# Kernel optimization log

Hardware: AMD Instinct MI355X
Metric: run time of the kernel (lower is better)

The kernel has to match this reference:

```python
import jax, jax.numpy as jnp
import numpy as np

AUDIO_DIM = 256
VIDEO_DIM = 256
CONV_CH = 128
FUSED_DIM = 512
EPS = 1e-12


def _interp_linear(x, t_out):
    # x: [B, T_in, D]; torch F.interpolate(mode='linear', align_corners=False)
    t_in = x.shape[1]
    scale = t_in / t_out
    src = (jnp.arange(t_out, dtype=jnp.float32) + 0.5) * scale - 0.5
    src = jnp.maximum(src, 0.0)
    i0 = jnp.floor(src).astype(jnp.int32)
    i0 = jnp.minimum(i0, t_in - 1)
    i1 = jnp.minimum(i0 + 1, t_in - 1)
    w = (src - i0.astype(jnp.float32))[None, :, None]
    return x[:, i0, :] * (1.0 - w) + x[:, i1, :] * w


def _conv1d(x, w, b, pad):
    # x: [B, C, T], w: [O, I, K]
    y = jax.lax.conv_general_dilated(x, w, window_strides=(1,), padding=[(pad, pad)],
                                     dimension_numbers=('NCH', 'OIH', 'NCH'))
    return y + b[None, :, None]


def setup_inputs() -> dict:
    key = jax.random.key(0)
    ks = jax.random.split(key, 12)
    B, Ta, Tv = 16, 2048, 1024

    def xavier(k, shape):
        fan_out, fan_in = shape[0], int(np.prod(shape[1:]))
        std = float(np.sqrt(2.0 / (fan_in + fan_out)))
        return jax.random.normal(k, shape, dtype=jnp.float32) * std

    return {
        'audio_features': jax.random.normal(ks[0], (B, Ta, AUDIO_DIM), dtype=jnp.float32),
        'video_features': jax.random.normal(ks[1], (B, Tv, VIDEO_DIM), dtype=jnp.float32),
        'a3_w': xavier(ks[2], (CONV_CH, AUDIO_DIM, 3)), 'a3_b': jnp.zeros((CONV_CH,), jnp.float32),
        'a5_w': xavier(ks[3], (CONV_CH, AUDIO_DIM, 5)), 'a5_b': jnp.zeros((CONV_CH,), jnp.float32),
        'v3_w': xavier(ks[4], (CONV_CH, VIDEO_DIM, 3)), 'v3_b': jnp.zeros((CONV_CH,), jnp.float32),
        'v5_w': xavier(ks[5], (CONV_CH, VIDEO_DIM, 5)), 'v5_b': jnp.zeros((CONV_CH,), jnp.float32),
        'proj_w': xavier(ks[6], (FUSED_DIM, FUSED_DIM)), 'proj_b': jnp.zeros((FUSED_DIM,), jnp.float32),
    }


def reference(audio_features, video_features, a3_w, a3_b, a5_w, a5_b,
              v3_w, v3_b, v5_w, v5_b, proj_w, proj_b):
    Ta, Tv = audio_features.shape[1], video_features.shape[1]
    T = max((Ta + Tv) // 2, 1)
    # temporal alignment to common length T
    a = _interp_linear(audio_features, T)  # [B, T, 256]
    v = _interp_linear(video_features, T)  # [B, T, 256]

    gelu = lambda x: jax.nn.gelu(x, approximate=False)
    a_in = jnp.swapaxes(a, 1, 2)  # [B, 256, T]
    v_in = jnp.swapaxes(v, 1, 2)
    a_multi = jnp.concatenate([gelu(_conv1d(a_in, a3_w, a3_b, 1)),
                               gelu(_conv1d(a_in, a5_w, a5_b, 2))], axis=1)  # [B, 256, T]
    v_multi = jnp.concatenate([gelu(_conv1d(v_in, v3_w, v3_b, 1)),
                               gelu(_conv1d(v_in, v5_w, v5_b, 2))], axis=1)
    a_multi = jnp.swapaxes(a_multi, 1, 2)  # [B, T, 256]
    v_multi = jnp.swapaxes(v_multi, 1, 2)

    # cosine-similarity cross attention (torch F.normalize eps=1e-12)
    a_norm = a_multi / jnp.maximum(jnp.linalg.norm(a_multi, axis=-1, keepdims=True), EPS)
    v_norm = v_multi / jnp.maximum(jnp.linalg.norm(v_multi, axis=-1, keepdims=True), EPS)
    sim = jnp.einsum('btd,bsd->bts', a_norm, v_norm)  # [B, T, T]

    attn_a2v = jax.nn.softmax(sim, axis=-1)              # audio attends video
    attn_v2a = jnp.swapaxes(jax.nn.softmax(sim, axis=1), 1, 2)  # video attends audio
    a_enh = jnp.einsum('bts,bsd->btd', attn_a2v, v_multi)
    v_enh = jnp.einsum('bst,btd->bsd', jnp.swapaxes(attn_v2a, 1, 2), a_multi)
    # (equivalently v_enh = attn_v2a @ a_multi)
    v_enh = jnp.einsum('bts,bsd->btd', attn_v2a, a_multi)

    fused = jnp.concatenate([a + a_enh, v + v_enh], axis=-1)  # [B, T, 512]
    out = gelu(fused @ proj_w.T + proj_b)
    # dropout is identity in eval mode
    return out
```

## Files before the change

### kernel.cpp

```cpp
#include <hip/hip_runtime.h>
#include <math.h>

#define BATCH 16
#define TA 2048
#define TV 1024
#define TT 1536
#define DIM 256
#define FD 512

typedef unsigned short u16;
typedef unsigned int u32;
typedef short bf16x8 __attribute__((ext_vector_type(8)));
typedef float f32x4 __attribute__((ext_vector_type(4)));

__device__ __forceinline__ float bf2f(u16 u) {
  union { u32 i; float f; } v; v.i = ((u32)u) << 16; return v.f;
}
__device__ __forceinline__ u16 f2bf(float f) {
  union { float f; u32 i; } v; v.f = f;
  return (u16)((v.i + 0x7fffu + ((v.i >> 16) & 1u)) >> 16);
}
__device__ __forceinline__ float gelu_f(float x) {
  return 0.5f * x * (1.0f + erff(x * 0.70710678118654752440f));
}
__device__ __forceinline__ void async16(const u16* g, u16* l) {
  __builtin_amdgcn_global_load_lds((const __attribute__((address_space(1))) void*)g,
                                   (__attribute__((address_space(3))) void*)l, 16, 0, 0);
}

__global__ __launch_bounds__(256) void k_prep(
    const float* __restrict__ a3w, const float* __restrict__ a5w,
    const float* __restrict__ v3w, const float* __restrict__ v5w,
    const float* __restrict__ pw,
    u16* __restrict__ w3a, u16* __restrict__ w5a,
    u16* __restrict__ w3v, u16* __restrict__ w5v, u16* __restrict__ wp) {
  int idx = blockIdx.x * 256 + threadIdx.x;
  if (idx < 524288) {
    int e, ktaps;
    const float* src;
    u16* dst;
    if (idx < 98304)       { e = idx;          ktaps = 3; src = a3w; dst = w3a; }
    else if (idx < 262144) { e = idx - 98304;  ktaps = 5; src = a5w; dst = w5a; }
    else if (idx < 360448) { e = idx - 262144; ktaps = 3; src = v3w; dst = w3v; }
    else                   { e = idx - 360448; ktaps = 5; src = v5w; dst = w5v; }
    int kk = e >> 12, r = e & 4095;
    int j = r & 7, unit = r >> 3;
    int fb = unit >> 6, rem = unit & 63;
    int q = rem >> 4, colp = rem & 15;
    int o = fb * 16 + colp;
    int tap = kk >> 3;
    int c = (kk & 7) * 32 + q * 8 + j;
    dst[e] = f2bf(src[(o * 256 + c) * ktaps + tap]);
  } else if (idx < 786432) {
    int t = idx - 524288;
    wp[t] = f2bf(pw[t]);
  }
}

__global__ __launch_bounds__(256) void k_interp(const float* __restrict__ in,
                                                u16* __restrict__ out,
                                                int t_in, float scale) {
  int b = blockIdx.y;
  int i = blockIdx.x * 256 + threadIdx.x;
  int t = i >> 5, dg = i & 31;
  float src = ((float)t + 0.5f) * scale - 0.5f;
  src = fmaxf(src, 0.0f);
  int i0 = (int)floorf(src);
  if (i0 > t_in - 1) i0 = t_in - 1;
  int i1 = i0 + 1; if (i1 > t_in - 1) i1 = t_in - 1;
  float w = src - (float)i0;
  float om = 1.0f - w;
  const float4* p0 = (const float4*)(in + ((size_t)(b * t_in + i0)) * DIM + dg * 8);
  const float4* p1 = (const float4*)(in + ((size_t)(b * t_in + i1)) * DIM + dg * 8);
  float4 x0a = p0[0], x0b = p0[1], x1a = p1[0], x1b = p1[1];
  u16 r[8];
  r[0] = f2bf(x0a.x * om + x1a.x * w); r[1] = f2bf(x0a.y * om + x1a.y * w);
  r[2] = f2bf(x0a.z * om + x1a.z * w); r[3] = f2bf(x0a.w * om + x1a.w * w);
  r[4] = f2bf(x0b.x * om + x1b.x * w); r[5] = f2bf(x0b.y * om + x1b.y * w);
  r[6] = f2bf(x0b.z * om + x1b.z * w); r[7] = f2bf(x0b.w * om + x1b.w * w);
  u32 w0 = (u32)r[0] | ((u32)r[1] << 16), w1 = (u32)r[2] | ((u32)r[3] << 16);
  u32 w2 = (u32)r[4] | ((u32)r[5] << 16), w3 = (u32)r[6] | ((u32)r[7] << 16);
  *(uint4*)(out + ((size_t)(b * TT + t)) * DIM + dg * 8) = make_uint4(w0, w1, w2, w3);
}

__global__ __launch_bounds__(256) void k_zero(float* __restrict__ p, int n) {
  int i = blockIdx.x * 256 + threadIdx.x;
  if (i < n) p[i] = 0.f;
}

template <int TAPS>
__global__ __launch_bounds__(256) void k_convN(
    const u16* __restrict__ xa, const u16* __restrict__ xv,
    const u16* __restrict__ Wa, const u16* __restrict__ Wv,
    const float* __restrict__ ba, const float* __restrict__ bv,
    u16* __restrict__ outMa, u16* __restrict__ outMv,
    u16* __restrict__ outTa, u16* __restrict__ outTv,
    float* __restrict__ nsqa, float* __restrict__ nsqv) {
  constexpr int S = TAPS * 8;
  constexpr int OFF = (TAPS == 3) ? 1 : 2;
  constexpr int CHB = (TAPS == 3) ? 0 : 128;
  __shared__ __align__(16) u16 xs[68 * 264];
  __shared__ __align__(16) u16 Bs[2 * 4096];
  u16* tb = xs;
  int b = blockIdx.y, t0 = blockIdx.x * 64;
  int isv = blockIdx.z;
  const u16* xin = isv ? xv : xa;
  const u16* W   = isv ? Wv : Wa;
  const float* bias = isv ? bv : ba;
  u16* outM  = isv ? outMv : outMa;
  u16* outT  = isv ? outTv : outTa;
  float* nsq = isv ? nsqv : nsqa;
  int tid = threadIdx.x, wave = tid >> 6, lane = tid & 63;
  int col = lane & 15, quad = lane >> 4;

  for (int i = tid; i < 68 * 32; i += 256) {
    int row = i >> 5, un = i & 31;
    int t = t0 + row - 2;
    uint4 val = make_uint4(0, 0, 0, 0);
    if (t >= 0 && t < TT) val = *(const uint4*)(xin + ((size_t)(b * TT + t)) * DIM + un * 8);
    *(uint4*)(xs + row * 264 + un * 8) = val;
  }
  const u16* Wb = W + wave * 1024 + lane * 8;
  u16* BsW = Bs + wave * 1024;
  async16(Wb, BsW);
  async16(Wb + 512, BsW + 512);

  f32x4 acc[4][2];
  f32x4 zz = {0.f, 0.f, 0.f, 0.f};
#pragma unroll
  for (int rt = 0; rt < 4; rt++) { acc[rt][0] = zz; acc[rt][1] = zz; }

  const u16* afp = xs + (col + 2) * 264 + quad * 8;
  const u16* bfp = Bs + wave * 1024 + quad * 128 + col * 8;

#pragma unroll
  for (int s = 0; s < S; s++) {
    __syncthreads();
    if (s + 1 < S) {
      const u16* src = Wb + (size_t)(s + 1) * 4096;
      u16* dst = Bs + ((s + 1) & 1) * 4096 + wave * 1024;
      async16(src, dst);
      async16(src + 512, dst + 512);
    }
    constexpr int dummy = 0; (void)dummy;
    int shift = (s >> 3) - OFF;
    int c0 = (s & 7) * 32;
    bf16x8 af[4];
#pragma unroll
    for (int rt = 0; rt < 4; rt++)
      af[rt] = *(const bf16x8*)(afp + (rt * 16 + shift) * 264 + c0);
    bf16x8 bf0 = *(const bf16x8*)(bfp + (s & 1) * 4096);
    bf16x8 bf1 = *(const bf16x8*)(bfp + (s & 1) * 4096 + 512);
#pragma unroll
    for (int rt = 0; rt < 4; rt++) {
      acc[rt][0] = __builtin_amdgcn_mfma_f32_16x16x32_bf16(af[rt], bf0, acc[rt][0], 0, 0, 0);
      acc[rt][1] = __builtin_amdgcn_mfma_f32_16x16x32_bf16(af[rt], bf1, acc[rt][1], 0, 0, 0);
    }
  }
  __syncthreads();

  float bia0 = bias[wave * 32 + col];
  float bia1 = bias[wave * 32 + 16 + col];
  float ss[4][4];
#pragma unroll
  for (int rt = 0; rt < 4; rt++)
#pragma unroll
    for (int r = 0; r < 4; r++) ss[rt][r] = 0.f;
#pragma unroll
  for (int rt = 0; rt < 4; rt++)
#pragma unroll
    for (int h = 0; h < 2; h++) {
      float bia = h ? bia1 : bia0;
      int chL = wave * 32 + h * 16 + col;
#pragma unroll
      for (int r = 0; r < 4; r++) {
        float g = gelu_f(acc[rt][h][r] + bia);
        ss[rt][r] += g * g;
        int trow = rt * 16 + quad * 4 + r;
        u16 gb = f2bf(g);
        tb[chL * 72 + trow] = gb;
        outM[((size_t)(b * TT + t0 + trow)) * DIM + CHB + chL] = gb;
      }
    }
#pragma unroll
  for (int rt = 0; rt < 4; rt++)
#pragma unroll
    for (int r = 0; r < 4; r++) {
      float v = ss[rt][r];
      v += __shfl_xor(v, 1, 64); v += __shfl_xor(v, 2, 64);
      v += __shfl_xor(v, 4, 64); v += __shfl_xor(v, 8, 64);
      if (col == 0)
        atomicAdd(&nsq[b * TT + t0 + rt * 16 + quad * 4 + r], v);
    }
  __syncthreads();
  {
    int ch = tid >> 1, half = tid & 1;
    uint4* dst = (uint4*)(outT + ((size_t)(b * 256 + CHB + ch)) * TT + t0 + half * 32);
#pragma unroll
    for (int i = 0; i < 4; i++)
      dst[i] = *(const uint4*)(tb + ch * 72 + half * 32 + i * 8);
  }
}

__global__ __launch_bounds__(256) void k_sim(const u16* __restrict__ A,
                                             const u16* __restrict__ Bm,
                                             const float* __restrict__ naq,
                                             const float* __restrict__ nvq,
                                             u16* __restrict__ E,
                                             u16* __restrict__ ET,
                                             float* __restrict__ rsum,
                                             float* __restrict__ csum) {
  __shared__ u16 As[128 * 32], Bs[128 * 32];
  __shared__ float sRa[128], sRv[128];
  int b = blockIdx.z, m0 = blockIdx.y * 128, n0 = blockIdx.x * 128;
  int tid = threadIdx.x, wave = tid >> 6, lane = tid & 63;
  int col = lane & 15, quad = lane >> 4;
  int wm = (wave >> 1) * 64, wn = (wave & 1) * 64;
  int lrow = lane >> 2, lcol = (lane & 3) * 8;
  if (tid < 128) sRa[tid] = 1.0f / fmaxf(sqrtf(naq[b * TT + m0 + tid]), 1e-12f);
  else sRv[tid - 128] = 1.0f / fmaxf(sqrtf(nvq[b * TT + tid - 128 + n0]), 1e-12f);
  const u16* Ab = A + ((size_t)(b * TT + m0)) * DIM;
  const u16* Bb = Bm + ((size_t)(b * TT + n0)) * DIM;
  f32x4 acc[4][4];
  f32x4 zz = {0.f, 0.f, 0.f, 0.f};
#pragma unroll
  for (int i = 0; i < 4; i++)
#pragma unroll
    for (int j = 0; j < 4; j++) acc[i][j] = zz;

  for (int kt = 0; kt < 8; kt++) {
    int k0 = kt * 32;
    __syncthreads();
#pragma unroll
    for (int i = 0; i < 2; i++) {
      int rb = wave * 32 + i * 16;
      async16(Ab + ((size_t)(rb + lrow)) * DIM + k0 + lcol, As + rb * 32);
      async16(Bb + ((size_t)(rb + lrow)) * DIM + k0 + lcol, Bs + rb * 32);
    }
    __syncthreads();
    bf16x8 af[4], bfr[4];
#pragma unroll
    for (int mt = 0; mt < 4; mt++) af[mt] = *(const bf16x8*)(As + (wm + mt * 16 + col) * 32 + quad * 8);
#pragma unroll
    for (int nt = 0; nt < 4; nt++) bfr[nt] = *(const bf16x8*)(Bs + (wn + nt * 16 + col) * 32 + quad * 8);
#pragma unroll
    for (int mt = 0; mt < 4; mt++)
#pragma unroll
      for (int nt = 0; nt < 4; nt++)
        acc[mt][nt] = __builtin_amdgcn_mfma_f32_16x16x32_bf16(af[mt], bfr[nt], acc[mt][nt], 0, 0, 0);
  }

  float rowp[4][4];
#pragma unroll
  for (int mt = 0; mt < 4; mt++)
#pragma unroll
    for (int r = 0; r < 4; r++) rowp[mt][r] = 0.f;

#pragma unroll
  for (int nt = 0; nt < 4; nt++) {
    int cl = wn + nt * 16 + col;
    float rv = sRv[cl];
    float colp = 0.f;
#pragma unroll
    for (int mt = 0; mt < 4; mt++) {
      u16 er[4];
#pragma unroll
      for (int r = 0; r < 4; r++) {
        int rl = wm + mt * 16 + quad * 4 + r;
        float e = __expf(acc[mt][nt][r] * sRa[rl] * rv);
        er[r] = f2bf(e);
        rowp[mt][r] += e;
        colp += e;
        E[((size_t)(b * TT + m0 + rl)) * TT + n0 + cl] = er[r];
      }
      u32 lo = (u32)er[0] | ((u32)er[1] << 16);
      u32 hi = (u32)er[2] | ((u32)er[3] << 16);
      *(uint2*)(ET + ((size_t)(b * TT + n0 + cl)) * TT + m0 + wm + mt * 16 + quad * 4) =
          make_uint2(lo, hi);
    }
    colp += __shfl_xor(colp, 16, 64);
    colp += __shfl_xor(colp, 32, 64);
    if (quad == 0) atomicAdd(&csum[b * TT + n0 + cl], colp);
  }
#pragma unroll
  for (int mt = 0; mt < 4; mt++)
#pragma unroll
    for (int r = 0; r < 4; r++) {
      float v = rowp[mt][r];
      v += __shfl_xor(v, 1, 64); v += __shfl_xor(v, 2, 64);
      v += __shfl_xor(v, 4, 64); v += __shfl_xor(v, 8, 64);
      if (col == 0) atomicAdd(&rsum[b * TT + m0 + wm + mt * 16 + quad * 4 + r], v);
    }
}

__global__ __launch_bounds__(256) void k_pv(
    const u16* __restrict__ P, const u16* __restrict__ Bt,
    const float* __restrict__ dsum,
    const u16* __restrict__ itp, u16* __restrict__ fused, int dstoff) {
  __shared__ u16 As[64 * 32];
  __shared__ u16 Bs[128 * 32];
  __shared__ float sSum[64];
  int b = blockIdx.z, m0 = blockIdx.y * 64, n0 = blockIdx.x * 128;
  int tid = threadIdx.x, wave = tid >> 6, lane = tid & 63;
  int col = lane & 15, quad = lane >> 4;
  int wm = (wave >> 1) * 32, wn = (wave & 1) * 64;
  int lrow = lane >> 2, lcol = (lane & 3) * 8;
  if (tid < 64) sSum[tid] = dsum[b * TT + m0 + tid];
  const u16* Ab = P + ((size_t)(b * TT + m0)) * TT;
  const u16* Bb = Bt + ((size_t)(b * 256 + n0)) * TT;
  f32x4 acc[2][4];
  f32x4 zz = {0.f, 0.f, 0.f, 0.f};
#pragma unroll
  for (int i = 0; i < 2; i++)
#pragma unroll
    for (int j = 0; j < 4; j++) acc[i][j] = zz;

  for (int kt = 0; kt < 48; kt++) {
    int k0 = kt * 32;
    __syncthreads();
    async16(Ab + ((size_t)(wave * 16 + lrow)) * TT + k0 + lcol, As + wave * 16 * 32);
#pragma unroll
    for (int i = 0; i < 2; i++) {
      int rb = wave * 32 + i * 16;
      async16(Bb + ((size_t)(rb + lrow)) * TT + k0 + lcol, Bs + rb * 32);
    }
    __syncthreads();
    bf16x8 af[2], bfr[4];
#pragma unroll
    for (int mt = 0; mt < 2; mt++) af[mt] = *(const bf16x8*)(As + (wm + mt * 16 + col) * 32 + quad * 8);
#pragma unroll
    for (int nt = 0; nt < 4; nt++) bfr[nt] = *(const bf16x8*)(Bs + (wn + nt * 16 + col) * 32 + quad * 8);
#pragma unroll
    for (int mt = 0; mt < 2; mt++)
#pragma unroll
      for (int nt = 0; nt < 4; nt++)
        acc[mt][nt] = __builtin_amdgcn_mfma_f32_16x16x32_bf16(af[mt], bfr[nt], acc[mt][nt], 0, 0, 0);
  }
#pragma unroll
  for (int mt = 0; mt < 2; mt++)
#pragma unroll
    for (int nt = 0; nt < 4; nt++)
#pragma unroll
      for (int r = 0; r < 4; r++) {
        int row = wm + mt * 16 + quad * 4 + r;
        int t = m0 + row;
        int d = n0 + wn + nt * 16 + col;
        float val = acc[mt][nt][r] / sSum[row] + bf2f(itp[((size_t)(b * TT + t)) * DIM + d]);
        fused[((size_t)(b * TT + t)) * FD + dstoff + d] = f2bf(val);
      }
}

__global__ __launch_bounds__(256) void k_proj(const u16* __restrict__ Am,
                                              const u16* __restrict__ Bw,
                                              const float* __restrict__ bias,
                                              float* __restrict__ out) {
  __shared__ u16 As[128 * 32], Bs[128 * 32];
  int m0 = blockIdx.y * 128, n0 = blockIdx.x * 128;
  int tid = threadIdx.x, wave = tid >> 6, lane = tid & 63;
  int col = lane & 15, quad = lane >> 4;
  int wm = (wave >> 1) * 64, wn = (wave & 1) * 64;
  int lrow = lane >> 2, lcol = (lane & 3) * 8;
  const u16* Ab = Am + (size_t)m0 * FD;
  const u16* Bb = Bw + (size_t)n0 * FD;
  f32x4 acc[4][4];
  f32x4 zz = {0.f, 0.f, 0.f, 0.f};
#pragma unroll
  for (int i = 0; i < 4; i++)
#pragma unroll
    for (int j = 0; j < 4; j++) acc[i][j] = zz;

  for (int kt = 0; kt < 16; kt++) {
    int k0 = kt * 32;
    __syncthreads();
#pragma unroll
    for (int i = 0; i < 2; i++) {
      int rb = wave * 32 + i * 16;
      async16(Ab + ((size_t)(rb + lrow)) * FD + k0 + lcol, As + rb * 32);
      async16(Bb + ((size_t)(rb + lrow)) * FD + k0 + lcol, Bs + rb * 32);
    }
    __syncthreads();
    bf16x8 af[4], bfr[4];
#pragma unroll
    for (int mt = 0; mt < 4; mt++) af[mt] = *(const bf16x8*)(As + (wm + mt * 16 + col) * 32 + quad * 8);
#pragma unroll
    for (int nt = 0; nt < 4; nt++) bfr[nt] = *(const bf16x8*)(Bs + (wn + nt * 16 + col) * 32 + quad * 8);
#pragma unroll
    for (int mt = 0; mt < 4; mt++)
#pragma unroll
      for (int nt = 0; nt < 4; nt++)
        acc[mt][nt] = __builtin_amdgcn_mfma_f32_16x16x32_bf16(af[mt], bfr[nt], acc[mt][nt], 0, 0, 0);
  }
#pragma unroll
  for (int nt = 0; nt < 4; nt++) {
    float bia = bias[n0 + wn + nt * 16 + col];
#pragma unroll
    for (int mt = 0; mt < 4; mt++)
#pragma unroll
      for (int r = 0; r < 4; r++) {
        int row = m0 + wm + mt * 16 + quad * 4 + r;
        int cc = n0 + wn + nt * 16 + col;
        out[(size_t)row * FD + cc] = gelu_f(acc[mt][nt][r] + bia);
      }
  }
}

extern "C" void kernel_launch(void* const* d_in, const int* in_sizes, int n_in,
                              void* d_out, int out_size, void* d_ws, size_t ws_size,
                              hipStream_t stream) {
  const float* audio = (const float*)d_in[0];
  const float* video = (const float*)d_in[1];
  const float* a3w = (const float*)d_in[2];
  const float* a3b = (const float*)d_in[3];
  const float* a5w = (const float*)d_in[4];
  const float* a5b = (const float*)d_in[5];
  const float* v3w = (const float*)d_in[6];
  const float* v3b = (const float*)d_in[7];
  const float* v5w = (const float*)d_in[8];
  const float* v5b = (const float*)d_in[9];
  const float* pw  = (const float*)d_in[10];
  const float* pb  = (const float*)d_in[11];
  float* out = (float*)d_out;

  char* ws = (char*)d_ws;
  size_t off = 0;
  auto alloc = [&](size_t bytes) {
    char* p = ws + off;
    off += (bytes + 255) & ~(size_t)255;
    return p;
  };
  size_t szItp = (size_t)BATCH * TT * DIM * 2;
  u16* a_itp = (u16*)alloc(szItp);
  u16* v_itp = (u16*)alloc(szItp);
  u16* aM  = (u16*)alloc(szItp);
  u16* vM  = (u16*)alloc(szItp);
  u16* aMT = (u16*)alloc(szItp);
  u16* vMT = (u16*)alloc(szItp);
  u16* E   = (u16*)alloc((size_t)BATCH * TT * TT * 2);
  u16* ET  = (u16*)alloc((size_t)BATCH * TT * TT * 2);
  float* naq = (float*)alloc((size_t)BATCH * TT * 4);
  float* nvq = (float*)alloc((size_t)BATCH * TT * 4);
  float* rsum = (float*)alloc((size_t)BATCH * TT * 4);
  float* csum = (float*)alloc((size_t)BATCH * TT * 4);
  u16* fusedb = (u16*)alloc((size_t)BATCH * TT * FD * 2);
  u16* w3a = (u16*)alloc(3 * 128 * 256 * 2);
  u16* w5a = (u16*)alloc(5 * 128 * 256 * 2);
  u16* w3v = (u16*)alloc(3 * 128 * 256 * 2);
  u16* w5v = (u16*)alloc(5 * 128 * 256 * 2);
  u16* wp  = (u16*)alloc(512 * 512 * 2);

  k_prep<<<3072, 256, 0, stream>>>(a3w, a5w, v3w, v5w, pw, w3a, w5a, w3v, w5v, wp);
  k_interp<<<dim3(192, 16), 256, 0, stream>>>(audio, a_itp, TA, (float)((double)TA / TT));
  k_interp<<<dim3(192, 16), 256, 0, stream>>>(video, v_itp, TV, (float)((double)TV / TT));
  k_zero<<<384, 256, 0, stream>>>(naq, 4 * BATCH * TT);
  k_convN<3><<<dim3(24, 16, 2), 256, 0, stream>>>(a_itp, v_itp, w3a, w3v, a3b, v3b,
                                                  aM, vM, aMT, vMT, naq, nvq);
  k_convN<5><<<dim3(24, 16, 2), 256, 0, stream>>>(a_itp, v_itp, w5a, w5v, a5b, v5b,
                                                  aM, vM, aMT, vMT, naq, nvq);
  k_sim<<<dim3(12, 12, 16), 256, 0, stream>>>(aM, vM, naq, nvq, E, ET, rsum, csum);
  k_pv<<<dim3(2, 24, 16), 256, 0, stream>>>(E, vMT, rsum, a_itp, fusedb, 0);
  k_pv<<<dim3(2, 24, 16), 256, 0, stream>>>(ET, aMT, csum, v_itp, fusedb, 256);
  k_proj<<<dim3(4, 192), 256, 0, stream>>>(fusedb, wp, pb, out);
}
```

Before: 380.6 us.

## Fuse similarity, softmax and PV into a flash-style kernel without materialising E

```diff
diff --git a/kernel.cpp b/kernel.cpp
--- a/kernel.cpp
+++ b/kernel.cpp
@@ -142,7 +142,6 @@
       async16(src, dst);
       async16(src + 512, dst + 512);
     }
-    constexpr int dummy = 0; (void)dummy;
     int shift = (s >> 3) - OFF;
     int c0 = (s & 7) * 32;
     bf16x8 af[4];
@@ -202,152 +201,169 @@
   }
 }
 
-__global__ __launch_bounds__(256) void k_sim(const u16* __restrict__ A,
-                                             const u16* __restrict__ Bm,
-                                             const float* __restrict__ naq,
-                                             const float* __restrict__ nvq,
-                                             u16* __restrict__ E,
-                                             u16* __restrict__ ET,
-                                             float* __restrict__ rsum,
-                                             float* __restrict__ csum) {
-  __shared__ u16 As[128 * 32], Bs[128 * 32];
-  __shared__ float sRa[128], sRv[128];
-  int b = blockIdx.z, m0 = blockIdx.y * 128, n0 = blockIdx.x * 128;
-  int tid = threadIdx.x, wave = tid >> 6, lane = tid & 63;
+__global__ __launch_bounds__(256, 2) void k_flash(
+    const u16* __restrict__ aM, const u16* __restrict__ vM,
+    const u16* __restrict__ aMT, const u16* __restrict__ vMT,
+    const float* __restrict__ naq, const float* __restrict__ nvq,
+    const u16* __restrict__ a_itp, const u16* __restrict__ v_itp,
+    u16* __restrict__ fused) {
+  __shared__ __align__(16) u16 sKV[8 * 64 * 32];
+  __shared__ __align__(16) u16 sKT[2 * 256 * 32];
+  __shared__ __align__(16) u16 sE[2 * 32 * 64];
+  __shared__ float sRv[64];
+  __shared__ float sDen[2][64];
+
+  int wgid = blockIdx.x;
+  int xcd = wgid & 7, j = wgid >> 3;
+  int g = xcd + 8 * (j / 24);
+  int m0 = (j % 24) * 64;
+  int b = g & 15, z = g >> 4;
+  const u16* Q    = z ? vM : aM;
+  const u16* KV   = z ? aM : vM;
+  const u16* KVT  = z ? aMT : vMT;
+  const float* nq = z ? nvq : naq;
+  const float* nk = z ? naq : nvq;
+  const u16* itp  = z ? v_itp : a_itp;
+  int dstoff = z ? 256 : 0;
+
+  int tid = threadIdx.x, w = tid >> 6, lane = tid & 63;
+  int mg = w >> 1, ng = w & 1;
   int col = lane & 15, quad = lane >> 4;
-  int wm = (wave >> 1) * 64, wn = (wave & 1) * 64;
-  int lrow = lane >> 2, lcol = (lane & 3) * 8;
-  if (tid < 128) sRa[tid] = 1.0f / fmaxf(sqrtf(naq[b * TT + m0 + tid]), 1e-12f);
-  else sRv[tid - 128] = 1.0f / fmaxf(sqrtf(nvq[b * TT + tid - 128 + n0]), 1e-12f);
-  const u16* Ab = A + ((size_t)(b * TT + m0)) * DIM;
-  const u16* Bb = Bm + ((size_t)(b * TT + n0)) * DIM;
-  f32x4 acc[4][4];
+  int li = lane >> 2;
+  int sq = (lane & 3) ^ ((lane >> 3) & 3);
+
+  bf16x8 qf[2][8];
+  const u16* Qb = Q + ((size_t)(b * TT + m0 + mg * 32)) * DIM;
+#pragma unroll
+  for (int mt = 0; mt < 2; mt++)
+#pragma unroll
+    for (int kt = 0; kt < 8; kt++)
+      qf[mt][kt] = *(const bf16x8*)(Qb + (size_t)(mt * 16 + col) * DIM + kt * 32 + quad * 8);
+
+  float sra[2][4];
+#pragma unroll
+  for (int mt = 0; mt < 2; mt++)
+#pragma unroll
+    for (int r = 0; r < 4; r++)
+      sra[mt][r] = 1.0f / fmaxf(
+          sqrtf(nq[(size_t)b * TT + m0 + mg * 32 + mt * 16 + quad * 4 + r]), 1e-12f);
+
+  f32x4 acc[2][8];
   f32x4 zz = {0.f, 0.f, 0.f, 0.f};
 #pragma unroll
-  for (int i = 0; i < 4; i++)
-#pragma unroll
-    for (int j = 0; j < 4; j++) acc[i][j] = zz;
-
-  for (int kt = 0; kt < 8; kt++) {
-    int k0 = kt * 32;
-    __syncthreads();
-#pragma unroll
-    for (int i = 0; i < 2; i++) {
-      int rb = wave * 32 + i * 16;
-      async16(Ab + ((size_t)(rb + lrow)) * DIM + k0 + lcol, As + rb * 32);
-      async16(Bb + ((size_t)(rb + lrow)) * DIM + k0 + lcol, Bs + rb * 32);
-    }
-    __syncthreads();
-    bf16x8 af[4], bfr[4];
-#pragma unroll
-    for (int mt = 0; mt < 4; mt++) af[mt] = *(const bf16x8*)(As + (wm + mt * 16 + col) * 32 + quad * 8);
-#pragma unroll
-    for (int nt = 0; nt < 4; nt++) bfr[nt] = *(const bf16x8*)(Bs + (wn + nt * 16 + col) * 32 + quad * 8);
-#pragma unroll
-    for (int mt = 0; mt < 4; mt++)
-#pragma unroll
-      for (int nt = 0; nt < 4; nt++)
-        acc[mt][nt] = __builtin_amdgcn_mfma_f32_16x16x32_bf16(af[mt], bfr[nt], acc[mt][nt], 0, 0, 0);
-  }
-
-  float rowp[4][4];
-#pragma unroll
-  for (int mt = 0; mt < 4; mt++)
-#pragma unroll
-    for (int r = 0; r < 4; r++) rowp[mt][r] = 0.f;
-
-#pragma unroll
-  for (int nt = 0; nt < 4; nt++) {
-    int cl = wn + nt * 16 + col;
-    float rv = sRv[cl];
-    float colp = 0.f;
-#pragma unroll
-    for (int mt = 0; mt < 4; mt++) {
-      u16 er[4];
-#pragma unroll
-      for (int r = 0; r < 4; r++) {
-        int rl = wm + mt * 16 + quad * 4 + r;
-        float e = __expf(acc[mt][nt][r] * sRa[rl] * rv);
-        er[r] = f2bf(e);
-        rowp[mt][r] += e;
-        colp += e;
-        E[((size_t)(b * TT + m0 + rl)) * TT + n0 + cl] = er[r];
-      }
-      u32 lo = (u32)er[0] | ((u32)er[1] << 16);
-      u32 hi = (u32)er[2] | ((u32)er[3] << 16);
-      *(uint2*)(ET + ((size_t)(b * TT + n0 + cl)) * TT + m0 + wm + mt * 16 + quad * 4) =
-          make_uint2(lo, hi);
-    }
-    colp += __shfl_xor(colp, 16, 64);
-    colp += __shfl_xor(colp, 32, 64);
-    if (quad == 0) atomicAdd(&csum[b * TT + n0 + cl], colp);
-  }
-#pragma unroll
-  for (int mt = 0; mt < 4; mt++)
+  for (int mt = 0; mt < 2; mt++)
+#pragma unroll
+    for (int dt = 0; dt < 8; dt++) acc[mt][dt] = zz;
+  float den[2][4];
+#pragma unroll
+  for (int mt = 0; mt < 2; mt++)
+#pragma unroll
+    for (int r = 0; r < 4; r++) den[mt][r] = 0.f;
+
+  const u16* KVb = KV + ((size_t)b * TT) * DIM;
+  const u16* KTb = KVT + ((size_t)b * 256) * TT;
+
+  for (int n0 = 0; n0 < TT; n0 += 64) {
+    __syncthreads();
+#pragma unroll
+    for (int kk = 0; kk < 2; kk++) {
+      int kt = w * 2 + kk;
+#pragma unroll
+      for (int i = 0; i < 4; i++) {
+        const u16* src = KVb + (size_t)(n0 + i * 16 + li) * DIM + kt * 32 + sq * 8;
+        async16(src, sKV + kt * 2048 + i * 512);
+      }
+    }
+#pragma unroll
+    for (int kn = 0; kn < 2; kn++)
+#pragma unroll
+      for (int i = 0; i < 4; i++) {
+        const u16* src = KTb + (size_t)(w * 64 + i * 16 + li) * TT + n0 + kn * 32 + sq * 8;
+        async16(src, sKT + kn * 8192 + w * 2048 + i * 512);
+      }
+    if (tid < 64)
+      sRv[tid] = 1.0f / fmaxf(sqrtf(nk[(size_t)b * TT + n0 + tid]), 1e-12f);
+    __syncthreads();
+
+    f32x4 sc[2][2];
+    sc[0][0] = zz; sc[0][1] = zz; sc[1][0] = zz; sc[1][1] = zz;
+#pragma unroll
+    for (int kt = 0; kt < 8; kt++)
+#pragma unroll
+      for (int nt = 0; nt < 2; nt++) {
+        int row = ng * 32 + nt * 16 + col;
+        bf16x8 bf = *(const bf16x8*)(sKV + kt * 2048 + row * 32 +
+                                     ((quad ^ ((row >> 1) & 3)) << 3));
+        sc[0][nt] = __builtin_amdgcn_mfma_f32_16x16x32_bf16(qf[0][kt], bf, sc[0][nt], 0, 0, 0);
+        sc[1][nt] = __builtin_amdgcn_mfma_f32_16x16x32_bf16(qf[1][kt], bf, sc[1][nt], 0, 0, 0);
+      }
+
+#pragma unroll
+    for (int mt = 0; mt < 2; mt++)
+#pragma unroll
+      for (int nt = 0; nt < 2; nt++) {
+        int c = ng * 32 + nt * 16 + col;
+        float rv = sRv[c];
+#pragma unroll
+        for (int r = 0; r < 4; r++) {
+          float e = __expf(sc[mt][nt][r] * sra[mt][r] * rv);
+          den[mt][r] += e;
+          int row = mt * 16 + quad * 4 + r;
+          sE[mg * 2048 + row * 64 + (((c >> 3) ^ ((row >> 1) & 7)) << 3) + (c & 7)] =
+              f2bf(e);
+        }
+      }
+    __syncthreads();
+
+#pragma unroll
+    for (int kn = 0; kn < 2; kn++) {
+      bf16x8 ea0, ea1;
+      {
+        int row = col;
+        ea0 = *(const bf16x8*)(sE + mg * 2048 + row * 64 +
+                               (((kn * 4 + quad) ^ ((row >> 1) & 7)) << 3));
+        row = 16 + col;
+        ea1 = *(const bf16x8*)(sE + mg * 2048 + row * 64 +
+                               (((kn * 4 + quad) ^ ((row >> 1) & 7)) << 3));
+      }
+#pragma unroll
+      for (int dt = 0; dt < 8; dt++) {
+        int drow = ng * 128 + dt * 16 + col;
+        bf16x8 bf = *(const bf16x8*)(sKT + kn * 8192 + drow * 32 +
+                                     ((quad ^ ((drow >> 1) & 3)) << 3));
+        acc[0][dt] = __builtin_amdgcn_mfma_f32_16x16x32_bf16(ea0, bf, acc[0][dt], 0, 0, 0);
+        acc[1][dt] = __builtin_amdgcn_mfma_f32_16x16x32_bf16(ea1, bf, acc[1][dt], 0, 0, 0);
+      }
+    }
+  }
+
+#pragma unroll
+  for (int mt = 0; mt < 2; mt++)
 #pragma unroll
     for (int r = 0; r < 4; r++) {
-      float v = rowp[mt][r];
+      float v = den[mt][r];
       v += __shfl_xor(v, 1, 64); v += __shfl_xor(v, 2, 64);
       v += __shfl_xor(v, 4, 64); v += __shfl_xor(v, 8, 64);
-      if (col == 0) atomicAdd(&rsum[b * TT + m0 + wm + mt * 16 + quad * 4 + r], v);
-    }
-}
-
-__global__ __launch_bounds__(256) void k_pv(
-    const u16* __restrict__ P, const u16* __restrict__ Bt,
-    const float* __restrict__ dsum,
-    const u16* __restrict__ itp, u16* __restrict__ fused, int dstoff) {
-  __shared__ u16 As[64 * 32];
-  __shared__ u16 Bs[128 * 32];
-  __shared__ float sSum[64];
-  int b = blockIdx.z, m0 = blockIdx.y * 64, n0 = blockIdx.x * 128;
-  int tid = threadIdx.x, wave = tid >> 6, lane = tid & 63;
-  int col = lane & 15, quad = lane >> 4;
-  int wm = (wave >> 1) * 32, wn = (wave & 1) * 64;
-  int lrow = lane >> 2, lcol = (lane & 3) * 8;
-  if (tid < 64) sSum[tid] = dsum[b * TT + m0 + tid];
-  const u16* Ab = P + ((size_t)(b * TT + m0)) * TT;
-  const u16* Bb = Bt + ((size_t)(b * 256 + n0)) * TT;
-  f32x4 acc[2][4];
-  f32x4 zz = {0.f, 0.f, 0.f, 0.f};
-#pragma unroll
-  for (int i = 0; i < 2; i++)
-#pragma unroll
-    for (int j = 0; j < 4; j++) acc[i][j] = zz;
-
-  for (int kt = 0; kt < 48; kt++) {
-    int k0 = kt * 32;
-    __syncthreads();
-    async16(Ab + ((size_t)(wave * 16 + lrow)) * TT + k0 + lcol, As + wave * 16 * 32);
-#pragma unroll
-    for (int i = 0; i < 2; i++) {
-      int rb = wave * 32 + i * 16;
-      async16(Bb + ((size_t)(rb + lrow)) * TT + k0 + lcol, Bs + rb * 32);
-    }
-    __syncthreads();
-    bf16x8 af[2], bfr[4];
-#pragma unroll
-    for (int mt = 0; mt < 2; mt++) af[mt] = *(const bf16x8*)(As + (wm + mt * 16 + col) * 32 + quad * 8);
-#pragma unroll
-    for (int nt = 0; nt < 4; nt++) bfr[nt] = *(const bf16x8*)(Bs + (wn + nt * 16 + col) * 32 + quad * 8);
-#pragma unroll
-    for (int mt = 0; mt < 2; mt++)
-#pragma unroll
-      for (int nt = 0; nt < 4; nt++)
-        acc[mt][nt] = __builtin_amdgcn_mfma_f32_16x16x32_bf16(af[mt], bfr[nt], acc[mt][nt], 0, 0, 0);
-  }
-#pragma unroll
-  for (int mt = 0; mt < 2; mt++)
-#pragma unroll
-    for (int nt = 0; nt < 4; nt++)
-#pragma unroll
-      for (int r = 0; r < 4; r++) {
-        int row = wm + mt * 16 + quad * 4 + r;
-        int t = m0 + row;
-        int d = n0 + wn + nt * 16 + col;
-        float val = acc[mt][nt][r] / sSum[row] + bf2f(itp[((size_t)(b * TT + t)) * DIM + d]);
-        fused[((size_t)(b * TT + t)) * FD + dstoff + d] = f2bf(val);
-      }
+      if (col == 0) sDen[ng][mg * 32 + mt * 16 + quad * 4 + r] = v;
+    }
+  __syncthreads();
+
+#pragma unroll
+  for (int mt = 0; mt < 2; mt++)
+#pragma unroll
+    for (int r = 0; r < 4; r++) {
+      int row = mg * 32 + mt * 16 + quad * 4 + r;
+      int t = m0 + row;
+      float dinv = 1.0f / (sDen[0][row] + sDen[1][row]);
+      const u16* ip = itp + ((size_t)(b * TT + t)) * DIM;
+      u16* op = fused + ((size_t)(b * TT + t)) * FD + dstoff;
+#pragma unroll
+      for (int dt = 0; dt < 8; dt++) {
+        int d = ng * 128 + dt * 16 + col;
+        float val = acc[mt][dt][r] * dinv + bf2f(ip[d]);
+        op[d] = f2bf(val);
+      }
+    }
 }
 
 __global__ __launch_bounds__(256) void k_proj(const u16* __restrict__ Am,
@@ -435,12 +451,8 @@
   u16* vM  = (u16*)alloc(szItp);
   u16* aMT = (u16*)alloc(szItp);
   u16* vMT = (u16*)alloc(szItp);
-  u16* E   = (u16*)alloc((size_t)BATCH * TT * TT * 2);
-  u16* ET  = (u16*)alloc((size_t)BATCH * TT * TT * 2);
   float* naq = (float*)alloc((size_t)BATCH * TT * 4);
   float* nvq = (float*)alloc((size_t)BATCH * TT * 4);
-  float* rsum = (float*)alloc((size_t)BATCH * TT * 4);
-  float* csum = (float*)alloc((size_t)BATCH * TT * 4);
   u16* fusedb = (u16*)alloc((size_t)BATCH * TT * FD * 2);
   u16* w3a = (u16*)alloc(3 * 128 * 256 * 2);
   u16* w5a = (u16*)alloc(5 * 128 * 256 * 2);
@@ -451,13 +463,11 @@
   k_prep<<<3072, 256, 0, stream>>>(a3w, a5w, v3w, v5w, pw, w3a, w5a, w3v, w5v, wp);
   k_interp<<<dim3(192, 16), 256, 0, stream>>>(audio, a_itp, TA, (float)((double)TA / TT));
   k_interp<<<dim3(192, 16), 256, 0, stream>>>(video, v_itp, TV, (float)((double)TV / TT));
-  k_zero<<<384, 256, 0, stream>>>(naq, 4 * BATCH * TT);
+  k_zero<<<192, 256, 0, stream>>>(naq, 2 * BATCH * TT);
   k_convN<3><<<dim3(24, 16, 2), 256, 0, stream>>>(a_itp, v_itp, w3a, w3v, a3b, v3b,
                                                   aM, vM, aMT, vMT, naq, nvq);
   k_convN<5><<<dim3(24, 16, 2), 256, 0, stream>>>(a_itp, v_itp, w5a, w5v, a5b, v5b,
                                                   aM, vM, aMT, vMT, naq, nvq);
-  k_sim<<<dim3(12, 12, 16), 256, 0, stream>>>(aM, vM, naq, nvq, E, ET, rsum, csum);
-  k_pv<<<dim3(2, 24, 16), 256, 0, stream>>>(E, vMT, rsum, a_itp, fusedb, 0);
-  k_pv<<<dim3(2, 24, 16), 256, 0, stream>>>(ET, aMT, csum, v_itp, fusedb, 256);
+  k_flash<<<768, 256, 0, stream>>>(aM, vM, aMT, vMT, naq, nvq, a_itp, v_itp, fusedb);
   k_proj<<<dim3(4, 192), 256, 0, stream>>>(fusedb, wp, pb, out);
 }
```

After: 352.9 us. 1.08x faster.
